# Kernel optimization log

Hardware: AMD Instinct MI355X
Metric: run time of the kernel (lower is better)

The kernel has to match this reference:

```python
import jax, jax.numpy as jnp
import numpy as np
import math

DIM = 512
HEADS = 8          # dim // num_head_channels = 512 // 64
HEAD_CH = 64
GROUPS = 32        # guided-diffusion normalization() = GroupNorm(32, dim)
EPS = 1e-5
CROSS_DIM = 768


def setup_inputs() -> dict:
    key = jax.random.key(0)
    ks = jax.random.split(key, 8)
    B, C, Hs, Ws, L = 16, DIM, 32, 32, 77
    x = jax.random.normal(ks[0], (B, C, Hs, Ws), dtype=jnp.float32)
    c = jax.random.normal(ks[1], (B, CROSS_DIM, L), dtype=jnp.float32)
    # GroupNorm affine params
    gamma = jnp.ones((C,), jnp.float32)
    beta = jnp.zeros((C,), jnp.float32)
    # 1x1 conv weights stored as [out, in]
    w_qkv = jax.random.normal(ks[2], (3 * C, C), jnp.float32) / math.sqrt(C)
    b_qkv = jnp.zeros((3 * C,), jnp.float32)
    w_c = jax.random.normal(ks[3], (2 * C, CROSS_DIM), jnp.float32) / math.sqrt(CROSS_DIM)
    b_c = jnp.zeros((2 * C,), jnp.float32)
    # NOTE: original proj_out is zero-initialized (zero_module); we use small
    # random weights so the reference exercises non-trivial math end-to-end.
    w_p = jax.random.normal(ks[4], (C, C), jnp.float32) / math.sqrt(C)
    b_p = jnp.zeros((C,), jnp.float32)
    return {"x": x, "c": c, "gamma": gamma, "beta": beta,
            "w_qkv": w_qkv, "b_qkv": b_qkv, "w_c": w_c, "b_c": b_c,
            "w_p": w_p, "b_p": b_p}


def reference(x, c, gamma, beta, w_qkv, b_qkv, w_c, b_c, w_p, b_p):
    B, C, Hs, Ws = x.shape
    T = Hs * Ws
    xf = x.reshape(B, C, T)

    # GroupNorm(32) over (channels_per_group, spatial)
    xg = xf.reshape(B, GROUPS, C // GROUPS, T)
    mean = xg.mean(axis=(2, 3), keepdims=True)
    var = xg.var(axis=(2, 3), keepdims=True)
    xn = ((xg - mean) * jax.lax.rsqrt(var + EPS)).reshape(B, C, T)
    xn = xn * gamma[None, :, None] + beta[None, :, None]

    # qkv 1x1 conv: [B, 3C, T]
    qkv = jnp.einsum('oc,bct->bot', w_qkv, xn) + b_qkv[None, :, None]
    q, k, v = jnp.split(qkv, 3, axis=1)
    q = q.reshape(B, HEADS, HEAD_CH, T)
    k = k.reshape(B, HEADS, HEAD_CH, T)
    v = v.reshape(B, HEADS, HEAD_CH, T)

    # cross-attn cond kv: [B, 2C, L] -> concat on sequence axis
    ckv = jnp.einsum('oc,bcl->bol', w_c, c) + b_c[None, :, None]
    kc, vc = jnp.split(ckv, 2, axis=1)
    L = c.shape[-1]
    k = jnp.concatenate([k, kc.reshape(B, HEADS, HEAD_CH, L)], axis=-1)
    v = jnp.concatenate([v, vc.reshape(B, HEADS, HEAD_CH, L)], axis=-1)

    scale = 1.0 / math.sqrt(HEAD_CH)
    # scores [B, H, T, T+L]; scale applied inside softmax as in FusedSoftmaxMaybeApex
    logits = jnp.einsum('bhct,bhcs->bhts', q, k) * scale
    w = jax.nn.softmax(logits, axis=-1)
    a = jnp.einsum('bhts,bhcs->bhct', w, v).reshape(B, C, T)

    h = jnp.einsum('oc,bct->bot', w_p, a) + b_p[None, :, None]
    return (xf + h).reshape(B, C, Hs, Ws)
```

## Files before the change

### kernel.cpp

```cpp
#include <hip/hip_runtime.h>

#define B_   16
#define C_   512
#define T_   1024
#define H_   8
#define D_   64
#define G_   32
#define L_   77
#define S_   1101
#define SPAD 1152
#define NPAD 51
#define CD_  768
#define BT_  (B_*T_)
#define SROW 72
#define QSC  0.18033688011112042f

typedef __bf16 bf16x8 __attribute__((ext_vector_type(8)));
typedef float  f32x4  __attribute__((ext_vector_type(4)));
typedef unsigned int u32x4 __attribute__((ext_vector_type(4)));

static __device__ __forceinline__ unsigned short f2bf(float f) {
    unsigned int u = __float_as_uint(f);
    u = (u + 0x7fffu + ((u >> 16) & 1u)) >> 16;
    return (unsigned short)u;
}

static __device__ __forceinline__ unsigned int pk_bf16(float a, float b) {
    unsigned int d;
    asm("v_cvt_pk_bf16_f32 %0, %1, %2" : "=v"(d) : "v"(a), "v"(b));
    return d;
}

static __device__ __forceinline__ void swap32(unsigned& a, unsigned& b) {
    asm volatile("v_permlane32_swap_b32 %0, %1" : "+v"(a), "+v"(b));
}
static __device__ __forceinline__ void swap16(unsigned& a, unsigned& b) {
    asm volatile("v_permlane16_swap_b32 %0, %1" : "+v"(a), "+v"(b));
}

static __device__ __forceinline__ void gload_lds16(const unsigned short* g,
                                                   unsigned short* l) {
    __builtin_amdgcn_global_load_lds(
        (const __attribute__((address_space(1))) unsigned int*)g,
        (__attribute__((address_space(3))) unsigned int*)l, 16, 0, 0);
}

__global__ __launch_bounds__(256) void prep_k(const float* __restrict__ x,
                                              float* __restrict__ stats,
                                              const float* __restrict__ w_qkv,
                                              const float* __restrict__ w_p,
                                              const float* __restrict__ w_c,
                                              const float* __restrict__ cin,
                                              unsigned short* __restrict__ wqkv_pk,
                                              unsigned short* __restrict__ wp_pk,
                                              unsigned short* __restrict__ wc_pk,
                                              unsigned short* __restrict__ cpk) {
    const int tid = threadIdx.x;
    if (blockIdx.x < 512) {
        const int bg = blockIdx.x;
        const float* p = x + (size_t)bg * 16384;
        float s = 0.f, s2 = 0.f;
        for (int i = tid; i < 16384; i += 256) {
            float v = p[i];
            s += v; s2 += v * v;
        }
        __shared__ float rs[256], rs2[256];
        rs[tid] = s; rs2[tid] = s2;
        __syncthreads();
        for (int off = 128; off > 0; off >>= 1) {
            if (tid < off) { rs[tid] += rs[tid + off]; rs2[tid] += rs2[tid + off]; }
            __syncthreads();
        }
        if (tid == 0) {
            float mean = rs[0] * (1.0f / 16384.0f);
            float var  = rs2[0] * (1.0f / 16384.0f) - mean * mean;
            stats[2 * bg]     = mean;
            stats[2 * bg + 1] = rsqrtf(var + 1e-5f);
        }
        return;
    }
    if (blockIdx.x < 1408) {
        const int cid = (blockIdx.x - 512) * 256 + tid;
        const float* src;
        unsigned short* dst;
        if (cid < 98304) {
            const int ml = cid & 127, k8 = (cid >> 7) & 7, kt = (cid >> 10) & 7, mt = cid >> 13;
            src = w_qkv + (size_t)(mt * 128 + ml) * 512 + kt * 64 + k8 * 8;
            dst = wqkv_pk + (size_t)cid * 8;
        } else if (cid < 131072) {
            const int c2 = cid - 98304;
            const int ml = c2 & 127, k8 = (c2 >> 7) & 7, kt = (c2 >> 10) & 7, mt = c2 >> 13;
            src = w_p + (size_t)(mt * 128 + ml) * 512 + kt * 64 + k8 * 8;
            dst = wp_pk + (size_t)c2 * 8;
        } else {
            const int c3 = cid - 131072;
            const int ml = c3 & 127, k8 = (c3 >> 7) & 7;
            const int ktmt = c3 >> 10;
            const int kt = ktmt % 12, mt = ktmt / 12;
            src = w_c + (size_t)(mt * 128 + ml) * 768 + kt * 64 + k8 * 8;
            dst = wc_pk + (size_t)c3 * 8;
        }
        const float4 v0 = *(const float4*)src, v1 = *(const float4*)(src + 4);
        unsigned short tmp[8];
        tmp[0] = f2bf(v0.x); tmp[1] = f2bf(v0.y); tmp[2] = f2bf(v0.z); tmp[3] = f2bf(v0.w);
        tmp[4] = f2bf(v1.x); tmp[5] = f2bf(v1.y); tmp[6] = f2bf(v1.z); tmp[7] = f2bf(v1.w);
        *(uint4*)dst = *(uint4*)tmp;
        return;
    }
    const int idx2 = blockIdx.x - 1408;
    const int kt = idx2 % 12, b = idx2 / 12;
#pragma unroll
    for (int it = 0; it < 4; it++) {
        const int idx = it * 256 + tid;
        const int k8 = idx >> 7, l = idx & 127;
        unsigned short tmp[8];
        const float* src = cin + ((size_t)b * CD_ + kt * 64 + k8 * 8) * L_ + l;
#pragma unroll
        for (int q = 0; q < 8; q++)
            tmp[q] = (l < L_) ? f2bf(src[(size_t)q * L_]) : (unsigned short)0;
        *(uint4*)&cpk[(size_t)b * 98304 + ((size_t)(kt * 8 + k8)) * 1024 + (size_t)l * 8] =
            *(uint4*)tmp;
    }
}

__global__ __launch_bounds__(256) void gn_apply_t(const float* __restrict__ x,
                                                  const float* __restrict__ stats,
                                                  const float* __restrict__ gamma,
                                                  const float* __restrict__ beta,
                                                  unsigned short* __restrict__ xnT) {
    const int t0 = blockIdx.x * 64, kt = blockIdx.y, b = blockIdx.z;
    const int c0 = kt * 64;
    const int tid = threadIdx.x;
    __shared__ float st[64][66];
#pragma unroll
    for (int it = 0; it < 4; it++) {
        const int fid = it * 256 + tid;
        const int ci = fid >> 4, t4 = (fid & 15) * 4;
        const int c = c0 + ci;
        const float4 xv = *(const float4*)&x[((size_t)(b * C_ + c) << 10) + t0 + t4];
        const int bg = b * G_ + (c >> 4);
        const float mean = stats[2 * bg], istd = stats[2 * bg + 1];
        const float gs = gamma[c] * istd, gb = beta[c] - mean * gs;
        st[t4 + 0][ci] = xv.x * gs + gb;
        st[t4 + 1][ci] = xv.y * gs + gb;
        st[t4 + 2][ci] = xv.z * gs + gb;
        st[t4 + 3][ci] = xv.w * gs + gb;
    }
    __syncthreads();
#pragma unroll
    for (int it = 0; it < 2; it++) {
        const int cid = it * 256 + tid;
        const int k8 = cid >> 6, tl = cid & 63;
        const int n = (b << 10) + t0 + tl;
        const int nt = n >> 7, nm = n & 127;
        unsigned short tmp[8];
        const float* src = &st[tl][k8 * 8];
#pragma unroll
        for (int q = 0; q < 8; q++) tmp[q] = f2bf(src[q]);
        *(uint4*)&xnT[(((size_t)nt * 8 + kt) * 8 + k8) * 1024 + (size_t)nm * 8] = *(uint4*)tmp;
    }
}

template<int MODE, int KT>
static __device__ __forceinline__ void mgemm_body(const unsigned short* __restrict__ Apk,
                                                  const unsigned short* __restrict__ Bpk,
                                                  const float* __restrict__ bias,
                                                  const float* __restrict__ resid,
                                                  unsigned short* __restrict__ qpk,
                                                  unsigned short* __restrict__ kpk,
                                                  unsigned short* __restrict__ vpk,
                                                  float* __restrict__ outp,
                                                  unsigned short* lds,
                                                  const int nt, const int mt, const int zz) {
    const int tid = threadIdx.x, wave = tid >> 6, lane = tid & 63;
    const int quad = lane >> 4, l16 = lane & 15;
    const int mw = (wave & 1) * 64, nw = (wave >> 1) * 64;

    f32x4 acc[4][4];
#pragma unroll
    for (int i = 0; i < 4; i++)
#pragma unroll
        for (int j = 0; j < 4; j++) acc[i][j] = (f32x4){0.f, 0.f, 0.f, 0.f};

    const unsigned short* Ab = Apk + (size_t)mt * KT * 8192;
    const unsigned short* Bb = Bpk + ((MODE == 2) ? (size_t)zz * KT * 8192 : 0)
                                   + (size_t)nt * KT * 8192;

    for (int kt = 0; kt < KT; kt++) {
        const unsigned short* as = Ab + kt * 8192 + wave * 2048 + lane * 8;
        const unsigned short* bs = Bb + kt * 8192 + wave * 2048 + lane * 8;
        unsigned short* la = lds + wave * 2048;
        unsigned short* lb = lds + 8192 + wave * 2048;
#pragma unroll
        for (int j = 0; j < 4; j++) {
            gload_lds16(as + j * 512, la + j * 512);
            gload_lds16(bs + j * 512, lb + j * 512);
        }
        __syncthreads();
#pragma unroll
        for (int kh = 0; kh < 2; kh++) {
            const int k8 = kh * 4 + quad;
            bf16x8 af[4], bfr[4];
#pragma unroll
            for (int i = 0; i < 4; i++) {
                af[i]  = *(const bf16x8*)&lds[(size_t)(k8 * 128 + mw + i * 16 + l16) * 8];
                bfr[i] = *(const bf16x8*)&lds[8192 + (size_t)(k8 * 128 + nw + i * 16 + l16) * 8];
            }
#pragma unroll
            for (int mi = 0; mi < 4; mi++)
#pragma unroll
                for (int ni = 0; ni < 4; ni++)
                    acc[mi][ni] = __builtin_amdgcn_mfma_f32_16x16x32_bf16(
                        af[mi], bfr[ni], acc[mi][ni], 0, 0, 0);
        }
        __syncthreads();
    }

    const int gm0 = mt * 128 + mw;
    const int gn0 = nt * 128 + nw;

    if (MODE == 1) {
        const int b = gn0 >> 10, t0 = gn0 & 1023;
#pragma unroll
        for (int mi = 0; mi < 4; mi++) {
#pragma unroll
            for (int r = 0; r < 4; r++) {
                const int m = gm0 + mi * 16 + quad * 4 + r;
                const float bv = bias[m];
                const size_t rowb = ((size_t)(b * C_ + m) << 10) + t0;
#pragma unroll
                for (int ni = 0; ni < 4; ni++) {
                    const size_t a = rowb + ni * 16 + l16;
                    outp[a] = acc[mi][ni][r] + bv + resid[a];
                }
            }
        }
        return;
    }

    const int region = gm0 >> 9;
    const int h = (gm0 & 511) >> 6;
    const int b = (MODE == 2) ? zz : (gn0 >> 10);
    const int bh = b * 8 + h;
    const bool vregion = (MODE == 0) ? (region == 2) : (region == 1);

    if (!vregion) {
        const float sc = (MODE == 0 && region == 0) ? QSC : 1.0f;
        unsigned short* base;
        int trow0;
        if (MODE == 0) {
            base = (region == 0) ? qpk + (size_t)bh * 16 * 4096
                                 : kpk + (size_t)bh * 18 * 4096;
            trow0 = gn0 & 1023;
        } else {
            base = kpk + (size_t)(bh * 18 + 16 + (gn0 >> 6)) * 4096;
            trow0 = -1;
        }
#pragma unroll
        for (int mi = 0; mi < 4; mi++) {
            const int k8 = mi * 2 + (quad >> 1);
            const int sub = (quad & 1) * 4;
#pragma unroll
            for (int ni = 0; ni < 4; ni++) {
                float vv[4];
                bool valid = true;
                if (MODE == 2) valid = (gn0 + ni * 16 + l16) < L_;
#pragma unroll
                for (int r = 0; r < 4; r++)
                    vv[r] = valid ? (acc[mi][ni][r] + bias[gm0 + mi * 16 + quad * 4 + r]) * sc
                                  : 0.f;
                uint2 d;
                d.x = pk_bf16(vv[0], vv[1]);
                d.y = pk_bf16(vv[2], vv[3]);
                unsigned short* dst;
                if (MODE == 0) {
                    const int t = trow0 + ni * 16 + l16;
                    dst = base + (size_t)(t >> 6) * 4096 + ((size_t)k8 * 64 + (t & 63)) * 8 + sub;
                } else {
                    const int row = ni * 16 + l16;
                    dst = base + ((size_t)k8 * 64 + row) * 8 + sub;
                }
                *(uint2*)dst = d;
            }
        }
    } else {
        unsigned short* wlds = lds + wave * 4608;
#pragma unroll
        for (int mi = 0; mi < 4; mi++)
#pragma unroll
            for (int ni = 0; ni < 4; ni++) {
                bool valid = true;
                if (MODE == 2) valid = (gn0 + ni * 16 + l16) < L_;
#pragma unroll
                for (int r = 0; r < 4; r++) {
                    const float v = valid ? acc[mi][ni][r] + bias[gm0 + mi * 16 + quad * 4 + r]
                                          : 0.f;
                    wlds[(mi * 16 + quad * 4 + r) * SROW + ni * 16 + l16] = f2bf(v);
                }
            }
        __syncthreads();
        const int stile = (MODE == 0) ? ((gn0 & 1023) >> 6) : (16 + (gn0 >> 6));
        unsigned short* dst = vpk + (size_t)(bh * 18 + stile) * 4096;
        const int sk8 = lane & 7, cb = lane >> 3;
#pragma unroll
        for (int it = 0; it < 8; it++) {
            const int ch = it * 8 + cb;
            *(uint4*)&dst[((size_t)sk8 * 64 + ch) * 8] =
                *(const uint4*)&wlds[ch * SROW + sk8 * 8];
        }
    }
}

__global__ __launch_bounds__(256) void mgemm_qkvc_k(const unsigned short* __restrict__ wqkv_pk,
                                                    const unsigned short* __restrict__ xnT,
                                                    const float* __restrict__ b_qkv,
                                                    const unsigned short* __restrict__ wc_pk,
                                                    const unsigned short* __restrict__ cpk,
                                                    const float* __restrict__ b_c,
                                                    unsigned short* __restrict__ qpk,
                                                    unsigned short* __restrict__ kpk,
                                                    unsigned short* __restrict__ vpk) {
    __shared__ unsigned short lds[18432];
    if (blockIdx.y < 12) {
        mgemm_body<0, 8>(wqkv_pk, xnT, b_qkv, nullptr, qpk, kpk, vpk, nullptr,
                         lds, blockIdx.x, blockIdx.y, 0);
    } else {
        mgemm_body<2, 12>(wc_pk, cpk, b_c, nullptr, nullptr, kpk, vpk, nullptr,
                          lds, 0, blockIdx.x & 7, blockIdx.x >> 3);
    }
}

__global__ __launch_bounds__(256) void mgemm_proj_k(const unsigned short* __restrict__ Apk,
                                                    const unsigned short* __restrict__ Bpk,
                                                    const float* __restrict__ bias,
                                                    const float* __restrict__ resid,
                                                    float* __restrict__ outp) {
    __shared__ unsigned short lds[18432];
    mgemm_body<1, 8>(Apk, Bpk, bias, resid, nullptr, nullptr, nullptr, outp,
                     lds, blockIdx.x, blockIdx.y, 0);
}

__global__ __launch_bounds__(256, 4) void flash_k(const unsigned short* __restrict__ qpk,
                                                  const unsigned short* __restrict__ kpk,
                                                  const unsigned short* __restrict__ vpk,
                                                  unsigned short* __restrict__ aT) {
    __shared__ __align__(16) unsigned short smem[16384];

    const int tid  = threadIdx.x;
    const int wave = tid >> 6, lane = tid & 63;
    const int quad = lane >> 4, l16 = lane & 15;
    const int bh  = blockIdx.x;
    const int b = bh >> 3, h = bh & 7;
    const int qt0 = blockIdx.y * 128;

    const unsigned short* qtb = qpk + ((size_t)bh * 16 + blockIdx.y * 2 + (wave >> 1)) * 4096;
    const int qr0 = (wave & 1) * 32 + l16;
    bf16x8 bq0[2], bq1[2];
#pragma unroll
    for (int s = 0; s < 2; s++) {
        bq0[s] = *(const bf16x8*)&qtb[((size_t)quad * 64 + qr0 + s * 16) * 8];
        bq1[s] = *(const bf16x8*)&qtb[((size_t)(quad + 4) * 64 + qr0 + s * 16) * 8];
    }

    const unsigned short* kbase = kpk + (size_t)bh * 18 * 4096 + wave * 1024 + lane * 8;
    const unsigned short* vbase = vpk + (size_t)bh * 18 * 4096 + wave * 1024 + lane * 8;

#define STAGE(p, t) do {                                                  \
        const unsigned short* kg = kbase + (size_t)(t) * 4096;            \
        const unsigned short* vg = vbase + (size_t)(t) * 4096;            \
        unsigned short* lkp = smem + (p) * 4096 + wave * 1024;            \
        unsigned short* lvp = smem + 8192 + (p) * 4096 + wave * 1024;     \
        gload_lds16(kg, lkp);       gload_lds16(kg + 512, lkp + 512);     \
        gload_lds16(vg, lvp);       gload_lds16(vg + 512, lvp + 512);     \
    } while (0)

    float rsum[2] = {0.f, 0.f};
    f32x4 o_acc[2][4];
#pragma unroll
    for (int s = 0; s < 2; s++)
#pragma unroll
        for (int nb = 0; nb < 4; nb++) o_acc[s][nb] = (f32x4){0.f, 0.f, 0.f, 0.f};

    STAGE(0, 0);
    __syncthreads();

    for (int t = 0; t < 18; t++) {
        const int p = t & 1;
        if (t < 17) STAGE(p ^ 1, t + 1);
        const unsigned short* kb = smem + p * 4096;
        const unsigned short* vb = smem + 8192 + p * 4096;

        f32x4 sacc[2][4];
#pragma unroll
        for (int sb = 0; sb < 4; sb++) {
            const bf16x8 ak0 = *(const bf16x8*)&kb[((size_t)quad * 64 + sb * 16 + l16) * 8];
            const bf16x8 ak1 = *(const bf16x8*)&kb[((size_t)(quad + 4) * 64 + sb * 16 + l16) * 8];
#pragma unroll
            for (int s = 0; s < 2; s++) {
                f32x4 z = (f32x4){0.f, 0.f, 0.f, 0.f};
                z = __builtin_amdgcn_mfma_f32_16x16x32_bf16(ak0, bq0[s], z, 0, 0, 0);
                z = __builtin_amdgcn_mfma_f32_16x16x32_bf16(ak1, bq1[s], z, 0, 0, 0);
                sacc[s][sb] = z;
            }
        }

        bf16x8 ap0[2], ap1[2];
#pragma unroll
        for (int s = 0; s < 2; s++) {
            unsigned w[4][2];
#pragma unroll
            for (int sb = 0; sb < 4; sb++) {
                const float e0 = __builtin_exp2f(sacc[s][sb][0]);
                const float e1 = __builtin_exp2f(sacc[s][sb][1]);
                const float e2 = __builtin_exp2f(sacc[s][sb][2]);
                const float e3 = __builtin_exp2f(sacc[s][sb][3]);
                rsum[s] += (e0 + e1) + (e2 + e3);
                w[sb][0] = pk_bf16(e0, e1);
                w[sb][1] = pk_bf16(e2, e3);
            }
            swap32(w[0][0], w[1][0]); swap16(w[0][0], w[1][0]);
            swap32(w[0][1], w[1][1]); swap16(w[0][1], w[1][1]);
            swap32(w[2][0], w[3][0]); swap16(w[2][0], w[3][0]);
            swap32(w[2][1], w[3][1]); swap16(w[2][1], w[3][1]);
            union { u32x4 u; bf16x8 v; } c0, c1;
            c0.u = (u32x4){w[0][0], w[0][1], w[1][0], w[1][1]};
            c1.u = (u32x4){w[2][0], w[2][1], w[3][0], w[3][1]};
            ap0[s] = c0.v;
            ap1[s] = c1.v;
        }

#pragma unroll
        for (int nb = 0; nb < 4; nb++) {
            const bf16x8 bv0 = *(const bf16x8*)&vb[((size_t)quad * 64 + nb * 16 + l16) * 8];
            const bf16x8 bv1 = *(const bf16x8*)&vb[((size_t)(quad + 4) * 64 + nb * 16 + l16) * 8];
#pragma unroll
            for (int s = 0; s < 2; s++) {
                o_acc[s][nb] = __builtin_amdgcn_mfma_f32_16x16x32_bf16(ap0[s], bv0, o_acc[s][nb], 0, 0, 0);
                o_acc[s][nb] = __builtin_amdgcn_mfma_f32_16x16x32_bf16(ap1[s], bv1, o_acc[s][nb], 0, 0, 0);
            }
        }
        __syncthreads();
    }
#undef STAGE

    float linv[2][4];
#pragma unroll
    for (int s = 0; s < 2; s++) {
        float lsum = rsum[s];
        lsum += __shfl_xor(lsum, 16);
        lsum += __shfl_xor(lsum, 32);
#pragma unroll
        for (int r = 0; r < 4; r++) {
            const float lr = __shfl(lsum, quad * 4 + r);
            linv[s][r] = 1.0f / (lr - (float)NPAD);
        }
    }

    unsigned short* ps = smem + wave * (32 * SROW);
#pragma unroll
    for (int s = 0; s < 2; s++)
#pragma unroll
        for (int nb = 0; nb < 4; nb++)
#pragma unroll
            for (int r = 0; r < 4; r++)
                ps[(s * 16 + quad * 4 + r) * SROW + nb * 16 + l16] =
                    f2bf(o_acc[s][nb][r] * linv[s][r]);
    asm volatile("s_waitcnt lgkmcnt(0)" ::: "memory");
    const int k8 = lane >> 3;
#pragma unroll
    for (int it = 0; it < 4; it++) {
        const int tl = (lane & 7) + it * 8;
        const int n = (b << 10) + qt0 + wave * 32 + tl;
        const int ntb = n >> 7, nm = n & 127;
        *(uint4*)&aT[(((size_t)ntb * 8 + h) * 8 + k8) * 1024 + (size_t)nm * 8] =
            *(const uint4*)&ps[tl * SROW + k8 * 8];
    }
}

extern "C" void kernel_launch(void* const* d_in, const int* in_sizes, int n_in,
                              void* d_out, int out_size, void* d_ws, size_t ws_size,
                              hipStream_t stream) {
    const float* x     = (const float*)d_in[0];
    const float* cin   = (const float*)d_in[1];
    const float* gamma = (const float*)d_in[2];
    const float* beta  = (const float*)d_in[3];
    const float* w_qkv = (const float*)d_in[4];
    const float* b_qkv = (const float*)d_in[5];
    const float* w_c   = (const float*)d_in[6];
    const float* b_c   = (const float*)d_in[7];
    const float* w_p   = (const float*)d_in[8];
    const float* b_p   = (const float*)d_in[9];
    float* out = (float*)d_out;

    float* ws    = (float*)d_ws;
    float* stats = ws;
    unsigned short* xnT     = (unsigned short*)(ws + 1024);
    unsigned short* wqkv_pk = xnT + 8388608;
    unsigned short* wp_pk   = wqkv_pk + 786432;
    unsigned short* wc_pk   = wp_pk + 262144;
    unsigned short* cpk     = wc_pk + 786432;
    unsigned short* qpk     = cpk + 1572864;
    unsigned short* kpk     = qpk + 8388608;
    unsigned short* vpk     = kpk + 9437184;
    unsigned short* aT      = vpk + 9437184;

    prep_k<<<dim3(1600), 256, 0, stream>>>(x, stats, w_qkv, w_p, w_c, cin,
                                           wqkv_pk, wp_pk, wc_pk, cpk);
    gn_apply_t<<<dim3(16, 8, 16), 256, 0, stream>>>(x, stats, gamma, beta, xnT);
    mgemm_qkvc_k<<<dim3(128, 13), 256, 0, stream>>>(wqkv_pk, xnT, b_qkv,
                                                    wc_pk, cpk, b_c,
                                                    qpk, kpk, vpk);
    flash_k<<<dim3(128, 8), 256, 0, stream>>>(qpk, kpk, vpk, aT);
    mgemm_proj_k<<<dim3(128, 4), 256, 0, stream>>>(wp_pk, aT, b_p, x, out);
}
```

Measured before the change: 266.6 us.

## Double-buffer GEMM K-tiles in LDS to overlap global loads with MFMA

```diff
diff --git a/kernel.cpp b/kernel.cpp
--- a/kernel.cpp
+++ b/kernel.cpp
@@ -29,6 +29,10 @@
     unsigned int d;
     asm("v_cvt_pk_bf16_f32 %0, %1, %2" : "=v"(d) : "v"(a), "v"(b));
     return d;
+}
+
+static __device__ __forceinline__ float exp2a(float x) {
+    return __builtin_exp2f(x);
 }
 
 static __device__ __forceinline__ void swap32(unsigned& a, unsigned& b) {
@@ -182,39 +186,42 @@
 #pragma unroll
         for (int j = 0; j < 4; j++) acc[i][j] = (f32x4){0.f, 0.f, 0.f, 0.f};
 
-    const unsigned short* Ab = Apk + (size_t)mt * KT * 8192;
+    const unsigned short* Ab = Apk + (size_t)mt * KT * 8192 + wave * 1024 + lane * 8;
     const unsigned short* Bb = Bpk + ((MODE == 2) ? (size_t)zz * KT * 8192 : 0)
-                                   + (size_t)nt * KT * 8192;
-
-    for (int kt = 0; kt < KT; kt++) {
-        const unsigned short* as = Ab + kt * 8192 + wave * 2048 + lane * 8;
-        const unsigned short* bs = Bb + kt * 8192 + wave * 2048 + lane * 8;
-        unsigned short* la = lds + wave * 2048;
-        unsigned short* lb = lds + 8192 + wave * 2048;
-#pragma unroll
-        for (int j = 0; j < 4; j++) {
-            gload_lds16(as + j * 512, la + j * 512);
-            gload_lds16(bs + j * 512, lb + j * 512);
-        }
+                                   + (size_t)nt * KT * 8192 + wave * 1024 + lane * 8;
+
+    const int NH = KT * 2;
+
+#define MSTAGE(p, h) do {                                                 \
+        const unsigned short* as = Ab + (size_t)(h) * 4096;               \
+        const unsigned short* bs = Bb + (size_t)(h) * 4096;               \
+        unsigned short* la = lds + (p) * 4096 + wave * 1024;              \
+        unsigned short* lb = lds + 8192 + (p) * 4096 + wave * 1024;       \
+        gload_lds16(as, la);        gload_lds16(as + 512, la + 512);      \
+        gload_lds16(bs, lb);        gload_lds16(bs + 512, lb + 512);      \
+    } while (0)
+
+    MSTAGE(0, 0);
+    __syncthreads();
+
+    for (int h = 0; h < NH; h++) {
+        const int p = h & 1;
+        if (h + 1 < NH) MSTAGE(p ^ 1, h + 1);
+        bf16x8 af[4], bfr[4];
+#pragma unroll
+        for (int i = 0; i < 4; i++) {
+            af[i]  = *(const bf16x8*)&lds[(size_t)(p * 4096) + (size_t)(quad * 128 + mw + i * 16 + l16) * 8];
+            bfr[i] = *(const bf16x8*)&lds[8192 + (size_t)(p * 4096) + (size_t)(quad * 128 + nw + i * 16 + l16) * 8];
+        }
+#pragma unroll
+        for (int mi = 0; mi < 4; mi++)
+#pragma unroll
+            for (int ni = 0; ni < 4; ni++)
+                acc[mi][ni] = __builtin_amdgcn_mfma_f32_16x16x32_bf16(
+                    af[mi], bfr[ni], acc[mi][ni], 0, 0, 0);
         __syncthreads();
-#pragma unroll
-        for (int kh = 0; kh < 2; kh++) {
-            const int k8 = kh * 4 + quad;
-            bf16x8 af[4], bfr[4];
-#pragma unroll
-            for (int i = 0; i < 4; i++) {
-                af[i]  = *(const bf16x8*)&lds[(size_t)(k8 * 128 + mw + i * 16 + l16) * 8];
-                bfr[i] = *(const bf16x8*)&lds[8192 + (size_t)(k8 * 128 + nw + i * 16 + l16) * 8];
-            }
-#pragma unroll
-            for (int mi = 0; mi < 4; mi++)
-#pragma unroll
-                for (int ni = 0; ni < 4; ni++)
-                    acc[mi][ni] = __builtin_amdgcn_mfma_f32_16x16x32_bf16(
-                        af[mi], bfr[ni], acc[mi][ni], 0, 0, 0);
-        }
-        __syncthreads();
-    }
+    }
+#undef MSTAGE
 
     const int gm0 = mt * 128 + mw;
     const int gn0 = nt * 128 + nw;
@@ -410,10 +417,10 @@
             unsigned w[4][2];
 #pragma unroll
             for (int sb = 0; sb < 4; sb++) {
-                const float e0 = __builtin_exp2f(sacc[s][sb][0]);
-                const float e1 = __builtin_exp2f(sacc[s][sb][1]);
-                const float e2 = __builtin_exp2f(sacc[s][sb][2]);
-                const float e3 = __builtin_exp2f(sacc[s][sb][3]);
+                const float e0 = exp2a(sacc[s][sb][0]);
+                const float e1 = exp2a(sacc[s][sb][1]);
+                const float e2 = exp2a(sacc[s][sb][2]);
+                const float e3 = exp2a(sacc[s][sb][3]);
                 rsum[s] += (e0 + e1) + (e2 + e3);
                 w[sb][0] = pk_bf16(e0, e1);
                 w[sb][1] = pk_bf16(e2, e3);
```

Result: no change. 268.3 us (+0.6%).
